# Optimization experiments

Measured on AMD Instinct MI355X. Metric: run time of the kernel, lower is better.

## Reference

```python
import jax, jax.numpy as jnp
import numpy as np

B, S = 2048, 256
V, E, H, LAT, NL = 4, 8, 64, 3, 2
NT = V + 2          # vocab + start + pad tokens
START = V
TEMP = 1.0


def setup_inputs() -> dict:
    key = jax.random.key(0)
    ks = jax.random.split(key, 32)
    def p(k, shape, scale=0.1):
        return jax.random.normal(k, shape, jnp.float32) * scale
    return {
        "tokens": jax.random.randint(ks[0], (B, S), 0, V),
        "emb": p(ks[1], (NT, E)),
        "enc_Wih0": p(ks[2], (3 * H, E)), "enc_Whh0": p(ks[3], (3 * H, H)),
        "enc_bih0": p(ks[4], (3 * H,)), "enc_bhh0": p(ks[5], (3 * H,)),
        "enc_Wih1": p(ks[6], (3 * H, H)), "enc_Whh1": p(ks[7], (3 * H, H)),
        "enc_bih1": p(ks[8], (3 * H,)), "enc_bhh1": p(ks[9], (3 * H,)),
        "fc_mu_W": p(ks[10], (LAT, H)), "fc_mu_b": p(ks[11], (LAT,)),
        "fc_var_W": p(ks[12], (LAT, H)), "fc_var_b": p(ks[13], (LAT,)),
        "dec_emb": p(ks[14], (NT, H)),
        "proj_W": p(ks[15], (H, LAT)), "proj_b": p(ks[16], (H,)),
        "dec_Wih0": p(ks[17], (3 * H, H)), "dec_Whh0": p(ks[18], (3 * H, H)),
        "dec_bih0": p(ks[19], (3 * H,)), "dec_bhh0": p(ks[20], (3 * H,)),
        "dec_Wih1": p(ks[21], (3 * H, H)), "dec_Whh1": p(ks[22], (3 * H, H)),
        "dec_bih1": p(ks[23], (3 * H,)), "dec_bhh1": p(ks[24], (3 * H,)),
        "head_W": p(ks[25], (V, H)), "head_b": p(ks[26], (V,)),
    }


def gru_cell(h, x, Wih, Whh, bih, bhh):
    # PyTorch GRU gate order: reset, update, new
    gi = x @ Wih.T + bih            # [B, 3H]
    gh = h @ Whh.T + bhh            # [B, 3H]
    ir, iz, ig = jnp.split(gi, 3, axis=-1)
    hr, hz, hg = jnp.split(gh, 3, axis=-1)
    r = jax.nn.sigmoid(ir + hr)
    z = jax.nn.sigmoid(iz + hz)
    n = jnp.tanh(ig + r * hg)
    return (1.0 - z) * n + z * h


def run_gru_layer(x, Wih, Whh, bih, bhh):
    # x: [B, S, D] -> (outputs [B, S, H], final hidden [B, H])
    def step(h, xt):
        h2 = gru_cell(h, xt, Wih, Whh, bih, bhh)
        return h2, h2
    h0 = jnp.zeros((x.shape[0], Whh.shape[1]), x.dtype)
    hT, ys = jax.lax.scan(step, h0, x.transpose(1, 0, 2))
    return ys.transpose(1, 0, 2), hT


def reference(tokens, emb, enc_Wih0, enc_Whh0, enc_bih0, enc_bhh0,
              enc_Wih1, enc_Whh1, enc_bih1, enc_bhh1,
              fc_mu_W, fc_mu_b, fc_var_W, fc_var_b,
              dec_emb, proj_W, proj_b,
              dec_Wih0, dec_Whh0, dec_bih0, dec_bhh0,
              dec_Wih1, dec_Whh1, dec_bih1, dec_bhh1,
              head_W, head_b):
    b, s = tokens.shape
    # ---- encode ----
    x = emb[tokens]                                   # [B, S, E]
    seq, _ = run_gru_layer(x, enc_Wih0, enc_Whh0, enc_bih0, enc_bhh0)
    _, h_last = run_gru_layer(seq, enc_Wih1, enc_Whh1, enc_bih1, enc_bhh1)
    mu = h_last @ fc_mu_W.T + fc_mu_b                 # [B, LAT]
    log_var = h_last @ fc_var_W.T + fc_var_b          # [B, LAT]
    # ---- reparameterize ----
    eps = jax.random.normal(jax.random.key(1), mu.shape, mu.dtype)
    z = eps * jnp.exp(0.5 * log_var) + mu
    hz = z @ proj_W.T + proj_b                        # [B, H]; same init for both layers
    tok0 = jnp.full((b,), START, jnp.int32)
    keys = jax.random.split(jax.random.key(2), s)
    def step(carry, k):
        h0, h1, tok = carry
        xe = dec_emb[tok]                             # [B, H]
        h0n = gru_cell(h0, xe, dec_Wih0, dec_Whh0, dec_bih0, dec_bhh0)
        h1n = gru_cell(h1, h0n, dec_Wih1, dec_Whh1, dec_bih1, dec_bhh1)
        logits = (h1n @ head_W.T + head_b) / TEMP     # [B, V]
        probs = jax.nn.softmax(logits, axis=-1)
        nt = jax.random.categorical(k, logits)        # multinomial sample (detached)
        return (h0n, h1n, nt), probs
    _, probs_seq = jax.lax.scan(step, (hz, hz, tok0), keys)   # [S, B, V]
    recons = probs_seq.transpose(1, 0, 2)[:, :, None, :]      # [B, S, 1, V]
    return recons, tokens, mu, log_var
```

## Files before the change

kernel.cpp:

```cpp
#include <hip/hip_runtime.h>
#include <stdint.h>

typedef unsigned int u32;
typedef unsigned short u16;

#define NB   2048
#define SS   256
#define HH   64
#define VV   4
#define LATD 3
#define NTHR 512

#define TOK_OFF (NB*SS*VV)
#define MU_OFF  (TOK_OFF + NB*SS)
#define LV_OFF  (MU_OFF + NB*LATD)

__device__ __forceinline__ void tf2x32(u32 k0, u32 k1, u32 x0, u32 x1, u32& o0, u32& o1){
  u32 k2 = k0 ^ k1 ^ 0x1BD11BDAu;
  x0 += k0; x1 += k1;
#define TFR(r) { x0 += x1; x1 = (x1<<r)|(x1>>(32-r)); x1 ^= x0; }
  TFR(13) TFR(15) TFR(26) TFR(6)   x0 += k1; x1 += k2 + 1u;
  TFR(17) TFR(29) TFR(16) TFR(24)  x0 += k2; x1 += k0 + 2u;
  TFR(13) TFR(15) TFR(26) TFR(6)   x0 += k0; x1 += k1 + 3u;
  TFR(17) TFR(29) TFR(16) TFR(24)  x0 += k1; x1 += k2 + 4u;
  TFR(13) TFR(15) TFR(26) TFR(6)   x0 += k2; x1 += k0 + 5u;
#undef TFR
  o0 = x0; o1 = x1;
}
__device__ __forceinline__ u32 foldb(u32 k0, u32 k1, u32 i){
  u32 a,b; tf2x32(k0,k1,0u,i,a,b); return a^b;
}
__device__ __forceinline__ float b2u(u32 bits){
  union{u32 i;float f;}c; c.i = (bits>>9) | 0x3f800000u; return c.f - 1.0f;
}
__device__ __forceinline__ float erfinv_f(float x){
  float w = -log1pf(-x*x);
  float p;
  if (w < 5.0f){
    w -= 2.5f;
    p = 2.81022636e-08f;
    p = fmaf(p,w, 3.43273939e-07f);
    p = fmaf(p,w,-3.5233877e-06f);
    p = fmaf(p,w,-4.39150654e-06f);
    p = fmaf(p,w, 0.00021858087f);
    p = fmaf(p,w,-0.00125372503f);
    p = fmaf(p,w,-0.00417768164f);
    p = fmaf(p,w, 0.246640727f);
    p = fmaf(p,w, 1.50140941f);
  } else {
    w = sqrtf(w) - 3.0f;
    p = -0.000200214257f;
    p = fmaf(p,w, 0.000100950558f);
    p = fmaf(p,w, 0.00134934322f);
    p = fmaf(p,w,-0.00367342844f);
    p = fmaf(p,w, 0.00573950773f);
    p = fmaf(p,w,-0.0076224613f);
    p = fmaf(p,w, 0.00943887047f);
    p = fmaf(p,w, 1.00167406f);
    p = fmaf(p,w, 2.83297682f);
  }
  return p*x;
}
__device__ __forceinline__ float sigm(float x){ return 1.0f/(1.0f+expf(-x)); }
__device__ __forceinline__ float rl(float x, int l){
  return __int_as_float(__builtin_amdgcn_readlane(__float_as_int(x), l));
}
__device__ __forceinline__ float wred(float x){
  #pragma unroll
  for (int m=1; m<64; m<<=1) x += __shfl_xor(x, m, 64);
  return x;
}

#define MATVEC1R(Wr, Wz, Wn, xv, ar, az, an)                                   \
  _Pragma("unroll")                                                            \
  for (int k4 = 0; k4 < 16; k4++){                                             \
    float4 wr = Wr[k4];                                                        \
    float4 wz = Wz[k4];                                                        \
    float4 wn = Wn[k4];                                                        \
    float x0 = rl(xv, 4*k4), x1 = rl(xv, 4*k4+1), x2 = rl(xv, 4*k4+2), x3 = rl(xv, 4*k4+3); \
    ar = fmaf(wr.x,x0,ar); ar = fmaf(wr.y,x1,ar); ar = fmaf(wr.z,x2,ar); ar = fmaf(wr.w,x3,ar); \
    az = fmaf(wz.x,x0,az); az = fmaf(wz.y,x1,az); az = fmaf(wz.z,x2,az); az = fmaf(wz.w,x3,az); \
    an = fmaf(wn.x,x0,an); an = fmaf(wn.y,x1,an); an = fmaf(wn.z,x2,an); an = fmaf(wn.w,x3,an); \
  }

#define MATVEC1L(W, xv, ar, az, an)                                            \
  _Pragma("unroll 2")                                                          \
  for (int k4 = 0; k4 < 16; k4++){                                             \
    float4 wr = W[k4*192 + j];                                                 \
    float4 wz = W[k4*192 + 64 + j];                                            \
    float4 wn = W[k4*192 + 128 + j];                                           \
    float x0 = rl(xv, 4*k4), x1 = rl(xv, 4*k4+1), x2 = rl(xv, 4*k4+2), x3 = rl(xv, 4*k4+3); \
    ar = fmaf(wr.x,x0,ar); ar = fmaf(wr.y,x1,ar); ar = fmaf(wr.z,x2,ar); ar = fmaf(wr.w,x3,ar); \
    az = fmaf(wz.x,x0,az); az = fmaf(wz.y,x1,az); az = fmaf(wz.z,x2,az); az = fmaf(wz.w,x3,az); \
    an = fmaf(wn.x,x0,an); an = fmaf(wn.y,x1,an); an = fmaf(wn.z,x2,an); an = fmaf(wn.w,x3,an); \
  }

#define LOAD_REG_W(G, Ar, Az, An)                                              \
  _Pragma("unroll")                                                            \
  for (int k4 = 0; k4 < 16; k4++){                                             \
    Ar[k4] = G[(j)*16 + k4];                                                   \
    Az[k4] = G[(64 + j)*16 + k4];                                              \
    An[k4] = G[(128 + j)*16 + k4];                                             \
  }

#define PIN4(v) asm volatile("" : "+v"(v.x), "+v"(v.y), "+v"(v.z), "+v"(v.w))
#define PIN_W(Ar, Az, An)                                                      \
  _Pragma("unroll")                                                            \
  for (int k4 = 0; k4 < 16; k4++){ PIN4(Ar[k4]); PIN4(Az[k4]); PIN4(An[k4]); }

__global__ __launch_bounds__(NTHR, 2) void enc_kernel(
    const int* __restrict__ tokens, const float* __restrict__ emb,
    const float* __restrict__ Wih0, const float* __restrict__ Whh0,
    const float* __restrict__ bih0, const float* __restrict__ bhh0,
    const float* __restrict__ Wih1, const float* __restrict__ Whh1,
    const float* __restrict__ bih1, const float* __restrict__ bhh1,
    const float* __restrict__ muW, const float* __restrict__ mub,
    const float* __restrict__ vaW, const float* __restrict__ vab,
    const float* __restrict__ pW,  const float* __restrict__ pb,
    float* __restrict__ out, float* __restrict__ hz_ws)
{
  __shared__ float4 wi1[16*192];
  __shared__ float4 wh1[16*192];
  __shared__ float tokT[VV*192];

  const int tid = threadIdx.x;
  const int b0  = blockIdx.x * 8;
  const int j   = tid & 63;
  const int wv  = tid >> 6;
  const int row = b0 + wv;

  for (int i4 = tid; i4 < 3072; i4 += NTHR){
    int g = i4 >> 4, k4 = i4 & 15;
    wi1[k4*192 + g] = ((const float4*)Wih1)[i4];
    wh1[k4*192 + g] = ((const float4*)Whh1)[i4];
  }
  if (tid < 192){
    #pragma unroll
    for (int v = 0; v < VV; v++){
      float acc = 0.0f;
      #pragma unroll
      for (int e = 0; e < 8; e++) acc = fmaf(emb[v*8+e], Wih0[tid*8+e], acc);
      tokT[v*192 + tid] = acc + bih0[tid];
    }
  }
  for (int i = tid; i < 8*SS; i += NTHR){
    int rr = i >> 8, tq = i & 255;
    out[TOK_OFF + (b0+rr)*SS + tq] = (float)tokens[(b0+rr)*SS + tq];
  }

  float4 w0r[16], w0z[16], w0n[16];
  {
    const float4* G0 = (const float4*)Whh0;
    LOAD_REG_W(G0, w0r, w0z, w0n)
    PIN_W(w0r, w0z, w0n)
  }
  __syncthreads();

  const float bhr0 = bhh0[j], bhz0 = bhh0[64+j], bhn0 = bhh0[128+j];
  const float bir1 = bih1[j], biz1 = bih1[64+j], bin1 = bih1[128+j];
  const float bhr1 = bhh1[j], bhz1 = bhh1[64+j], bhn1 = bhh1[128+j];

  float h0 = 0.0f, h1 = 0.0f;
  const int tR = row*SS;

  for (int t = 0; t < SS; t++){
    asm volatile("" ::: "memory");
    int k = tokens[tR + t];
    float ar=0, az=0, an=0;
    MATVEC1R(w0r, w0z, w0n, h0, ar, az, an)
    {
      float ir = tokT[k*192+j], iz = tokT[k*192+64+j], ig = tokT[k*192+128+j];
      float rg = sigm(ir + ar + bhr0);
      float zg = sigm(iz + az + bhz0);
      float ng = tanhf(ig + rg*(an + bhn0));
      h0 = (1.0f - zg)*ng + zg*h0;
    }
    float air=0, aiz=0, ain=0, ahr=0, ahz=0, ahn=0;
    MATVEC1L(wi1, h0, air, aiz, ain)
    MATVEC1L(wh1, h1, ahr, ahz, ahn)
    {
      float rg = sigm(air + bir1 + ahr + bhr1);
      float zg = sigm(aiz + biz1 + ahz + bhz1);
      float ng = tanhf(ain + bin1 + rg*(ahn + bhn1));
      h1 = (1.0f - zg)*ng + zg*h1;
    }
  }

  const float LO_ = -0.99999994f;
  {
    float hv = h1;
    int gb = row;
    float mu0,mu1,mu2, lv0,lv1,lv2;
    { float pm = muW[0*64+j]*hv; pm = wred(pm); mu0 = pm + mub[0];
      float pv = vaW[0*64+j]*hv; pv = wred(pv); lv0 = pv + vab[0]; }
    { float pm = muW[1*64+j]*hv; pm = wred(pm); mu1 = pm + mub[1];
      float pv = vaW[1*64+j]*hv; pv = wred(pv); lv1 = pv + vab[1]; }
    { float pm = muW[2*64+j]*hv; pm = wred(pm); mu2 = pm + mub[2];
      float pv = vaW[2*64+j]*hv; pv = wred(pv); lv2 = pv + vab[2]; }
    if (j < 3){
      float mv  = (j==0)?mu0:(j==1)?mu1:mu2;
      float lvv = (j==0)?lv0:(j==1)?lv1:lv2;
      out[MU_OFF + gb*LATD + j] = mv;
      out[LV_OFF + gb*LATD + j] = lvv;
    }
    float z0,z1,z2;
    #pragma unroll
    for (int l = 0; l < 3; l++){
      u32 bits = foldb(0u, 1u, (u32)(gb*LATD + l));
      float u01 = b2u(bits);
      float uu = u01 * 2.0f;
      uu = uu + LO_;
      uu = fmaxf(LO_, uu);
      float ep = 1.41421354f * erfinv_f(uu);
      float lvv = (l==0)?lv0:(l==1)?lv1:lv2;
      float mvv = (l==0)?mu0:(l==1)?mu1:mu2;
      float zv = ep * expf(0.5f*lvv) + mvv;
      if (l==0) z0 = zv; else if (l==1) z1 = zv; else z2 = zv;
    }
    float hzj = pW[j*3+0]*z0;
    hzj += pW[j*3+1]*z1;
    hzj += pW[j*3+2]*z2;
    hzj += pb[j];
    hz_ws[gb*HH + j] = hzj;
  }
}

__global__ __launch_bounds__(NTHR, 2) void dec_kernel(
    const float* __restrict__ demb,
    const float* __restrict__ Wih0, const float* __restrict__ Whh0,
    const float* __restrict__ bih0, const float* __restrict__ bhh0,
    const float* __restrict__ Wih1, const float* __restrict__ Whh1,
    const float* __restrict__ bih1, const float* __restrict__ bhh1,
    const float* __restrict__ headW, const float* __restrict__ headb,
    const float* __restrict__ hz_ws, float* __restrict__ out)
{
  __shared__ float4 wi1[16*192];
  __shared__ float4 wh1[16*192];
  __shared__ float decT[6*192];
  __shared__ u32 sk0[SS], sk1[SS];

  const int tid = threadIdx.x;
  const int b0  = blockIdx.x * 8;
  const int j   = tid & 63;
  const int wv  = tid >> 6;
  const int row = b0 + wv;

  for (int i4 = tid; i4 < 3072; i4 += NTHR){
    int g = i4 >> 4, k4 = i4 & 15;
    wi1[k4*192 + g] = ((const float4*)Wih1)[i4];
    wh1[k4*192 + g] = ((const float4*)Whh1)[i4];
  }
  if (tid < 192){
    #pragma unroll
    for (int v = 0; v < 6; v++){
      float acc = 0.0f;
      #pragma unroll 8
      for (int k = 0; k < 64; k++) acc = fmaf(demb[v*64+k], Wih0[tid*64+k], acc);
      decT[v*192 + tid] = acc + bih0[tid];
    }
  }
  if (tid < SS){
    u32 a,b; tf2x32(0u, 2u, 0u, (u32)tid, a, b);
    sk0[tid] = a; sk1[tid] = b;
  }

  float4 w0r[16], w0z[16], w0n[16];
  {
    const float4* G0 = (const float4*)Whh0;
    LOAD_REG_W(G0, w0r, w0z, w0n)
  }
  __syncthreads();

  const float bhr0 = bhh0[j], bhz0 = bhh0[64+j], bhn0 = bhh0[128+j];
  const float bir1 = bih1[j], biz1 = bih1[64+j], bin1 = bih1[128+j];
  const float bhr1 = bhh1[j], bhz1 = bhh1[64+j], bhn1 = bhh1[128+j];
  const float hw0 = headW[0*64+j], hw1 = headW[1*64+j], hw2 = headW[2*64+j], hw3 = headW[3*64+j];
  const float hb0 = headb[0], hb1 = headb[1], hb2 = headb[2], hb3 = headb[3];

  float h0 = hz_ws[row*HH + j];
  float h1 = h0;
  int tk = 4;

  const int vv = j & 3;
  const float TINY = 1.17549435e-38f;

  for (int t = 0; t < SS; t++){
    asm volatile("" ::: "memory");
    float ar=0, az=0, an=0;
    MATVEC1R(w0r, w0z, w0n, h0, ar, az, an)
    {
      float ir = decT[tk*192+j], iz = decT[tk*192+64+j], ig = decT[tk*192+128+j];
      float rg = sigm(ir + ar + bhr0);
      float zg = sigm(iz + az + bhz0);
      float ng = tanhf(ig + rg*(an + bhn0));
      h0 = (1.0f - zg)*ng + zg*h0;
    }
    float air=0, aiz=0, ain=0, ahr=0, ahz=0, ahn=0;
    MATVEC1L(wi1, h0, air, aiz, ain)
    MATVEC1L(wh1, h1, ahr, ahz, ahn)
    {
      float rg = sigm(air + bir1 + ahr + bhr1);
      float zg = sigm(aiz + biz1 + ahz + bhz1);
      float ng = tanhf(ain + bin1 + rg*(ahn + bhn1));
      h1 = (1.0f - zg)*ng + zg*h1;
    }
    float l0 = wred(hw0*h1) + hb0;
    float l1 = wred(hw1*h1) + hb1;
    float l2 = wred(hw2*h1) + hb2;
    float l3 = wred(hw3*h1) + hb3;
    float lg = (vv==0)?l0:(vv==1)?l1:(vv==2)?l2:l3;
    u32 bits = foldb(sk0[t], sk1[t], (u32)(row*VV + vv));
    float u01 = b2u(bits);
    float u = u01 + TINY;
    u = fmaxf(TINY, u);
    float gmb = -logf(-logf(u));
    float prt = lg + gmb;
    float mx = lg;
    mx = fmaxf(mx, __shfl_xor(mx, 1, 64));
    mx = fmaxf(mx, __shfl_xor(mx, 2, 64));
    float e = expf(lg - mx);
    float se = e;
    se += __shfl_xor(se, 1, 64);
    se += __shfl_xor(se, 2, 64);
    float prob = e / se;
    float bp = prt; int bv = vv;
    { float o = __shfl_xor(bp, 1, 64); int ov = __shfl_xor(bv, 1, 64);
      if (o > bp || (o == bp && ov < bv)){ bp = o; bv = ov; } }
    { float o = __shfl_xor(bp, 2, 64); int ov = __shfl_xor(bv, 2, 64);
      if (o > bp || (o == bp && ov < bv)){ bp = o; bv = ov; } }
    if (j < 4) out[(size_t)row*SS*VV + (size_t)t*VV + vv] = prob;
    tk = __builtin_amdgcn_readlane(bv, 0);
  }
}

extern "C" void kernel_launch(void* const* d_in, const int* in_sizes, int n_in,
                              void* d_out, int out_size, void* d_ws, size_t ws_size,
                              hipStream_t stream){
  const int*   tokens = (const int*)d_in[0];
  const float* emb    = (const float*)d_in[1];
  const float* eWih0  = (const float*)d_in[2];  const float* eWhh0 = (const float*)d_in[3];
  const float* ebih0  = (const float*)d_in[4];  const float* ebhh0 = (const float*)d_in[5];
  const float* eWih1  = (const float*)d_in[6];  const float* eWhh1 = (const float*)d_in[7];
  const float* ebih1  = (const float*)d_in[8];  const float* ebhh1 = (const float*)d_in[9];
  const float* muW    = (const float*)d_in[10]; const float* mub   = (const float*)d_in[11];
  const float* vaW    = (const float*)d_in[12]; const float* vab   = (const float*)d_in[13];
  const float* demb   = (const float*)d_in[14];
  const float* pW     = (const float*)d_in[15]; const float* pb    = (const float*)d_in[16];
  const float* dWih0  = (const float*)d_in[17]; const float* dWhh0 = (const float*)d_in[18];
  const float* dbih0  = (const float*)d_in[19]; const float* dbhh0 = (const float*)d_in[20];
  const float* dWih1  = (const float*)d_in[21]; const float* dWhh1 = (const float*)d_in[22];
  const float* dbih1  = (const float*)d_in[23]; const float* dbhh1 = (const float*)d_in[24];
  const float* hWp    = (const float*)d_in[25]; const float* hbp   = (const float*)d_in[26];
  float* out = (float*)d_out;
  float* hz = (float*)d_ws;

  enc_kernel<<<NB/8, NTHR, 0, stream>>>(tokens, emb,
      eWih0, eWhh0, ebih0, ebhh0, eWih1, eWhh1, ebih1, ebhh1,
      muW, mub, vaW, vab, pW, pb, out, hz);
  dec_kernel<<<NB/8, NTHR, 0, stream>>>(demb,
      dWih0, dWhh0, dbih0, dbhh0, dWih1, dWhh1, dbih1, dbhh1,
      hWp, hbp, hz, out);
}
```

Baseline: 2.632 ms.

## Split GRU matvecs across wave pairs by K-half, processing two rows per wave

Each pair of waves now handles two batch rows together. Each wave keeps only half of the layer-0 recurrent weights in registers and computes partial matvecs over its half of K. The partials are exchanged through shared memory with block-wide barriers, and in the decoder the sampled tokens are shared the same way. This halves register pressure for the pinned weights and reuses each weight load for two rows. In exchange it adds two __syncthreads per timestep plus extra LDS traffic and duplicated gate math.

```diff
diff --git a/kernel.cpp b/kernel.cpp
--- a/kernel.cpp
+++ b/kernel.cpp
@@ -2,7 +2,6 @@
 #include <stdint.h>
 
 typedef unsigned int u32;
-typedef unsigned short u16;
 
 #define NB   2048
 #define SS   256
@@ -71,42 +70,50 @@
   return x;
 }
 
-#define MATVEC1R(Wr, Wz, Wn, xv, ar, az, an)                                   \
+#define PIN4(v) asm volatile("" : "+v"(v.x), "+v"(v.y), "+v"(v.z), "+v"(v.w))
+#define PIN_W8(Ar, Az, An)                                                     \
   _Pragma("unroll")                                                            \
-  for (int k4 = 0; k4 < 16; k4++){                                             \
-    float4 wr = Wr[k4];                                                        \
-    float4 wz = Wz[k4];                                                        \
-    float4 wn = Wn[k4];                                                        \
-    float x0 = rl(xv, 4*k4), x1 = rl(xv, 4*k4+1), x2 = rl(xv, 4*k4+2), x3 = rl(xv, 4*k4+3); \
-    ar = fmaf(wr.x,x0,ar); ar = fmaf(wr.y,x1,ar); ar = fmaf(wr.z,x2,ar); ar = fmaf(wr.w,x3,ar); \
-    az = fmaf(wz.x,x0,az); az = fmaf(wz.y,x1,az); az = fmaf(wz.z,x2,az); az = fmaf(wz.w,x3,az); \
-    an = fmaf(wn.x,x0,an); an = fmaf(wn.y,x1,an); an = fmaf(wn.z,x2,an); an = fmaf(wn.w,x3,an); \
-  }
-
-#define MATVEC1L(W, xv, ar, az, an)                                            \
+  for (int k4 = 0; k4 < 8; k4++){ PIN4(Ar[k4]); PIN4(An[k4]); PIN4(Az[k4]); }
+
+#define MATVEC0P(hA, hB)                                                       \
+  _Pragma("unroll")                                                            \
+  for (int k4 = 0; k4 < 8; k4++){                                              \
+    float4 wr = w0r[k4], wz = w0z[k4], wn = w0n[k4];                           \
+    int kb = kb0 + 4*k4;                                                       \
+    float a0=rl(hA,kb), a1=rl(hA,kb+1), a2=rl(hA,kb+2), a3=rl(hA,kb+3);        \
+    float c0=rl(hB,kb), c1=rl(hB,kb+1), c2=rl(hB,kb+2), c3=rl(hB,kb+3);        \
+    arA=fmaf(wr.x,a0,arA); arA=fmaf(wr.y,a1,arA); arA=fmaf(wr.z,a2,arA); arA=fmaf(wr.w,a3,arA); \
+    azA=fmaf(wz.x,a0,azA); azA=fmaf(wz.y,a1,azA); azA=fmaf(wz.z,a2,azA); azA=fmaf(wz.w,a3,azA); \
+    anA=fmaf(wn.x,a0,anA); anA=fmaf(wn.y,a1,anA); anA=fmaf(wn.z,a2,anA); anA=fmaf(wn.w,a3,anA); \
+    arB=fmaf(wr.x,c0,arB); arB=fmaf(wr.y,c1,arB); arB=fmaf(wr.z,c2,arB); arB=fmaf(wr.w,c3,arB); \
+    azB=fmaf(wz.x,c0,azB); azB=fmaf(wz.y,c1,azB); azB=fmaf(wz.z,c2,azB); azB=fmaf(wz.w,c3,azB); \
+    anB=fmaf(wn.x,c0,anB); anB=fmaf(wn.y,c1,anB); anB=fmaf(wn.z,c2,anB); anB=fmaf(wn.w,c3,anB); \
+  }
+
+#define MATVEC1P(xA, xB, yA, yB)                                               \
   _Pragma("unroll 2")                                                          \
-  for (int k4 = 0; k4 < 16; k4++){                                             \
-    float4 wr = W[k4*192 + j];                                                 \
-    float4 wz = W[k4*192 + 64 + j];                                            \
-    float4 wn = W[k4*192 + 128 + j];                                           \
-    float x0 = rl(xv, 4*k4), x1 = rl(xv, 4*k4+1), x2 = rl(xv, 4*k4+2), x3 = rl(xv, 4*k4+3); \
-    ar = fmaf(wr.x,x0,ar); ar = fmaf(wr.y,x1,ar); ar = fmaf(wr.z,x2,ar); ar = fmaf(wr.w,x3,ar); \
-    az = fmaf(wz.x,x0,az); az = fmaf(wz.y,x1,az); az = fmaf(wz.z,x2,az); az = fmaf(wz.w,x3,az); \
-    an = fmaf(wn.x,x0,an); an = fmaf(wn.y,x1,an); an = fmaf(wn.z,x2,an); an = fmaf(wn.w,x3,an); \
-  }
-
-#define LOAD_REG_W(G, Ar, Az, An)                                              \
-  _Pragma("unroll")                                                            \
-  for (int k4 = 0; k4 < 16; k4++){                                             \
-    Ar[k4] = G[(j)*16 + k4];                                                   \
-    Az[k4] = G[(64 + j)*16 + k4];                                              \
-    An[k4] = G[(128 + j)*16 + k4];                                             \
-  }
-
-#define PIN4(v) asm volatile("" : "+v"(v.x), "+v"(v.y), "+v"(v.z), "+v"(v.w))
-#define PIN_W(Ar, Az, An)                                                      \
-  _Pragma("unroll")                                                            \
-  for (int k4 = 0; k4 < 16; k4++){ PIN4(Ar[k4]); PIN4(Az[k4]); PIN4(An[k4]); }
+  for (int k4 = 0; k4 < 8; k4++){                                              \
+    int ki = kh8 + k4;                                                         \
+    float4 wir = wi1[ki*192 + j],  wiz = wi1[ki*192 + 64 + j],  win = wi1[ki*192 + 128 + j]; \
+    float4 whr = wh1[ki*192 + j],  whz = wh1[ki*192 + 64 + j],  whn = wh1[ki*192 + 128 + j]; \
+    int kb = 4*ki;                                                             \
+    float xa0=rl(xA,kb), xa1=rl(xA,kb+1), xa2=rl(xA,kb+2), xa3=rl(xA,kb+3);    \
+    float xb0=rl(xB,kb), xb1=rl(xB,kb+1), xb2=rl(xB,kb+2), xb3=rl(xB,kb+3);    \
+    float ya0=rl(yA,kb), ya1=rl(yA,kb+1), ya2=rl(yA,kb+2), ya3=rl(yA,kb+3);    \
+    float yb0=rl(yB,kb), yb1=rl(yB,kb+1), yb2=rl(yB,kb+2), yb3=rl(yB,kb+3);    \
+    srA=fmaf(wir.x,xa0,srA); srA=fmaf(wir.y,xa1,srA); srA=fmaf(wir.z,xa2,srA); srA=fmaf(wir.w,xa3,srA); \
+    srA=fmaf(whr.x,ya0,srA); srA=fmaf(whr.y,ya1,srA); srA=fmaf(whr.z,ya2,srA); srA=fmaf(whr.w,ya3,srA); \
+    szA=fmaf(wiz.x,xa0,szA); szA=fmaf(wiz.y,xa1,szA); szA=fmaf(wiz.z,xa2,szA); szA=fmaf(wiz.w,xa3,szA); \
+    szA=fmaf(whz.x,ya0,szA); szA=fmaf(whz.y,ya1,szA); szA=fmaf(whz.z,ya2,szA); szA=fmaf(whz.w,ya3,szA); \
+    inA=fmaf(win.x,xa0,inA); inA=fmaf(win.y,xa1,inA); inA=fmaf(win.z,xa2,inA); inA=fmaf(win.w,xa3,inA); \
+    hnA=fmaf(whn.x,ya0,hnA); hnA=fmaf(whn.y,ya1,hnA); hnA=fmaf(whn.z,ya2,hnA); hnA=fmaf(whn.w,ya3,hnA); \
+    srB=fmaf(wir.x,xb0,srB); srB=fmaf(wir.y,xb1,srB); srB=fmaf(wir.z,xb2,srB); srB=fmaf(wir.w,xb3,srB); \
+    srB=fmaf(whr.x,yb0,srB); srB=fmaf(whr.y,yb1,srB); srB=fmaf(whr.z,yb2,srB); srB=fmaf(whr.w,yb3,srB); \
+    szB=fmaf(wiz.x,xb0,szB); szB=fmaf(wiz.y,xb1,szB); szB=fmaf(wiz.z,xb2,szB); szB=fmaf(wiz.w,xb3,szB); \
+    szB=fmaf(whz.x,yb0,szB); szB=fmaf(whz.y,yb1,szB); szB=fmaf(whz.z,yb2,szB); szB=fmaf(whz.w,yb3,szB); \
+    inB=fmaf(win.x,xb0,inB); inB=fmaf(win.y,xb1,inB); inB=fmaf(win.z,xb2,inB); inB=fmaf(win.w,xb3,inB); \
+    hnB=fmaf(whn.x,yb0,hnB); hnB=fmaf(whn.y,yb1,hnB); hnB=fmaf(whn.z,yb2,hnB); hnB=fmaf(whn.w,yb3,hnB); \
+  }
 
 __global__ __launch_bounds__(NTHR, 2) void enc_kernel(
     const int* __restrict__ tokens, const float* __restrict__ emb,
@@ -122,12 +129,22 @@
   __shared__ float4 wi1[16*192];
   __shared__ float4 wh1[16*192];
   __shared__ float tokT[VV*192];
+  __shared__ float4 ex1a[8][64];
+  __shared__ float2 ex1b[8][64];
+  __shared__ float4 ex2a[8][64];
+  __shared__ float4 ex2b[8][64];
 
   const int tid = threadIdx.x;
   const int b0  = blockIdx.x * 8;
   const int j   = tid & 63;
   const int wv  = tid >> 6;
-  const int row = b0 + wv;
+  const int kh  = wv & 1;
+  const int pw  = wv ^ 1;
+  const int rA  = b0 + (wv & ~1);
+  const int rB  = rA + 1;
+  const int rD  = b0 + wv;
+  const int kh8 = kh * 8;
+  const int kb0 = kh * 32;
 
   for (int i4 = tid; i4 < 3072; i4 += NTHR){
     int g = i4 >> 4, k4 = i4 & 15;
@@ -148,48 +165,77 @@
     out[TOK_OFF + (b0+rr)*SS + tq] = (float)tokens[(b0+rr)*SS + tq];
   }
 
-  float4 w0r[16], w0z[16], w0n[16];
+  float4 w0r[8], w0z[8], w0n[8];
   {
     const float4* G0 = (const float4*)Whh0;
-    LOAD_REG_W(G0, w0r, w0z, w0n)
-    PIN_W(w0r, w0z, w0n)
+    #pragma unroll
+    for (int k4 = 0; k4 < 8; k4++){
+      w0r[k4] = G0[(j)*16      + kh8 + k4];
+      w0z[k4] = G0[(64 + j)*16 + kh8 + k4];
+      w0n[k4] = G0[(128 + j)*16+ kh8 + k4];
+    }
+    PIN_W8(w0r, w0z, w0n)
   }
   __syncthreads();
 
   const float bhr0 = bhh0[j], bhz0 = bhh0[64+j], bhn0 = bhh0[128+j];
-  const float bir1 = bih1[j], biz1 = bih1[64+j], bin1 = bih1[128+j];
-  const float bhr1 = bhh1[j], bhz1 = bhh1[64+j], bhn1 = bhh1[128+j];
-
-  float h0 = 0.0f, h1 = 0.0f;
-  const int tR = row*SS;
+  const float bR1  = bih1[j]      + bhh1[j];
+  const float bZ1  = bih1[64+j]   + bhh1[64+j];
+  const float bin1 = bih1[128+j], bhn1 = bhh1[128+j];
+
+  float h0A = 0.0f, h0B = 0.0f, h1A = 0.0f, h1B = 0.0f;
 
   for (int t = 0; t < SS; t++){
     asm volatile("" ::: "memory");
-    int k = tokens[tR + t];
-    float ar=0, az=0, an=0;
-    MATVEC1R(w0r, w0z, w0n, h0, ar, az, an)
-    {
-      float ir = tokT[k*192+j], iz = tokT[k*192+64+j], ig = tokT[k*192+128+j];
-      float rg = sigm(ir + ar + bhr0);
-      float zg = sigm(iz + az + bhz0);
-      float ng = tanhf(ig + rg*(an + bhn0));
-      h0 = (1.0f - zg)*ng + zg*h0;
-    }
-    float air=0, aiz=0, ain=0, ahr=0, ahz=0, ahn=0;
-    MATVEC1L(wi1, h0, air, aiz, ain)
-    MATVEC1L(wh1, h1, ahr, ahz, ahn)
-    {
-      float rg = sigm(air + bir1 + ahr + bhr1);
-      float zg = sigm(aiz + biz1 + ahz + bhz1);
-      float ng = tanhf(ain + bin1 + rg*(ahn + bhn1));
-      h1 = (1.0f - zg)*ng + zg*h1;
+    int kA = tokens[rA*SS + t];
+    int kB = tokens[rB*SS + t];
+    float arA=0, azA=0, anA=0, arB=0, azB=0, anB=0;
+    MATVEC0P(h0A, h0B)
+    ex1a[wv][j] = make_float4(arA, azA, anA, arB);
+    ex1b[wv][j] = make_float2(azB, anB);
+    __syncthreads();
+    {
+      float4 qa = ex1a[pw][j]; float2 qb = ex1b[pw][j];
+      arA += qa.x; azA += qa.y; anA += qa.z;
+      arB += qa.w; azB += qb.x; anB += qb.y;
+    }
+    {
+      float ir = tokT[kA*192+j], iz = tokT[kA*192+64+j], ig = tokT[kA*192+128+j];
+      float rg = sigm(ir + arA + bhr0);
+      float zg = sigm(iz + azA + bhz0);
+      float ng = tanhf(ig + rg*(anA + bhn0));
+      h0A = (1.0f - zg)*ng + zg*h0A;
+    }
+    {
+      float ir = tokT[kB*192+j], iz = tokT[kB*192+64+j], ig = tokT[kB*192+128+j];
+      float rg = sigm(ir + arB + bhr0);
+      float zg = sigm(iz + azB + bhz0);
+      float ng = tanhf(ig + rg*(anB + bhn0));
+      h0B = (1.0f - zg)*ng + zg*h0B;
+    }
+    float srA=0, szA=0, inA=0, hnA=0, srB=0, szB=0, inB=0, hnB=0;
+    MATVEC1P(h0A, h0B, h1A, h1B)
+    ex2a[wv][j] = make_float4(srA, szA, inA, hnA);
+    ex2b[wv][j] = make_float4(srB, szB, inB, hnB);
+    __syncthreads();
+    {
+      float4 pa = ex2a[pw][j];
+      float rg = sigm(srA + pa.x + bR1);
+      float zg = sigm(szA + pa.y + bZ1);
+      float ng = tanhf(inA + pa.z + bin1 + rg*(hnA + pa.w + bhn1));
+      h1A = (1.0f - zg)*ng + zg*h1A;
+      float4 pb = ex2b[pw][j];
+      rg = sigm(srB + pb.x + bR1);
+      zg = sigm(szB + pb.y + bZ1);
+      ng = tanhf(inB + pb.z + bin1 + rg*(hnB + pb.w + bhn1));
+      h1B = (1.0f - zg)*ng + zg*h1B;
     }
   }
 
   const float LO_ = -0.99999994f;
   {
-    float hv = h1;
-    int gb = row;
+    float hv = kh ? h1B : h1A;
+    int gb = rD;
     float mu0,mu1,mu2, lv0,lv1,lv2;
     { float pm = muW[0*64+j]*hv; pm = wred(pm); mu0 = pm + mub[0];
       float pv = vaW[0*64+j]*hv; pv = wred(pv); lv0 = pv + vab[0]; }
@@ -238,12 +284,24 @@
   __shared__ float4 wh1[16*192];
   __shared__ float decT[6*192];
   __shared__ u32 sk0[SS], sk1[SS];
+  __shared__ int tokS[8];
+  __shared__ float4 ex1a[8][64];
+  __shared__ float2 ex1b[8][64];
+  __shared__ float4 ex2a[8][64];
+  __shared__ float4 ex2b[8][64];
 
   const int tid = threadIdx.x;
   const int b0  = blockIdx.x * 8;
   const int j   = tid & 63;
   const int wv  = tid >> 6;
-  const int row = b0 + wv;
+  const int kh  = wv & 1;
+  const int pw  = wv ^ 1;
+  const int rA  = b0 + (wv & ~1);
+  const int rB  = rA + 1;
+  const int rD  = b0 + wv;
+  const int kh8 = kh * 8;
+  const int kb0 = kh * 32;
+  const int pbase = wv & ~1;
 
   for (int i4 = tid; i4 < 3072; i4 += NTHR){
     int g = i4 >> 4, k4 = i4 & 15;
@@ -263,53 +321,87 @@
     u32 a,b; tf2x32(0u, 2u, 0u, (u32)tid, a, b);
     sk0[tid] = a; sk1[tid] = b;
   }
-
-  float4 w0r[16], w0z[16], w0n[16];
+  if (tid < 8) tokS[tid] = 4;
+
+  float4 w0r[8], w0z[8], w0n[8];
   {
     const float4* G0 = (const float4*)Whh0;
-    LOAD_REG_W(G0, w0r, w0z, w0n)
+    #pragma unroll
+    for (int k4 = 0; k4 < 8; k4++){
+      w0r[k4] = G0[(j)*16      + kh8 + k4];
+      w0z[k4] = G0[(64 + j)*16 + kh8 + k4];
+      w0n[k4] = G0[(128 + j)*16+ kh8 + k4];
+    }
+    PIN_W8(w0r, w0z, w0n)
   }
   __syncthreads();
 
   const float bhr0 = bhh0[j], bhz0 = bhh0[64+j], bhn0 = bhh0[128+j];
-  const float bir1 = bih1[j], biz1 = bih1[64+j], bin1 = bih1[128+j];
-  const float bhr1 = bhh1[j], bhz1 = bhh1[64+j], bhn1 = bhh1[128+j];
+  const float bR1  = bih1[j]      + bhh1[j];
+  const float bZ1  = bih1[64+j]   + bhh1[64+j];
+  const float bin1 = bih1[128+j], bhn1 = bhh1[128+j];
   const float hw0 = headW[0*64+j], hw1 = headW[1*64+j], hw2 = headW[2*64+j], hw3 = headW[3*64+j];
   const float hb0 = headb[0], hb1 = headb[1], hb2 = headb[2], hb3 = headb[3];
 
-  float h0 = hz_ws[row*HH + j];
-  float h1 = h0;
-  int tk = 4;
+  float h0A = hz_ws[rA*HH + j];
+  float h0B = hz_ws[rB*HH + j];
+  float h1A = h0A, h1B = h0B;
 
   const int vv = j & 3;
   const float TINY = 1.17549435e-38f;
 
   for (int t = 0; t < SS; t++){
     asm volatile("" ::: "memory");
-    float ar=0, az=0, an=0;
-    MATVEC1R(w0r, w0z, w0n, h0, ar, az, an)
-    {
-      float ir = decT[tk*192+j], iz = decT[tk*192+64+j], ig = decT[tk*192+128+j];
-      float rg = sigm(ir + ar + bhr0);
-      float zg = sigm(iz + az + bhz0);
-      float ng = tanhf(ig + rg*(an + bhn0));
-      h0 = (1.0f - zg)*ng + zg*h0;
-    }
-    float air=0, aiz=0, ain=0, ahr=0, ahz=0, ahn=0;
-    MATVEC1L(wi1, h0, air, aiz, ain)
-    MATVEC1L(wh1, h1, ahr, ahz, ahn)
-    {
-      float rg = sigm(air + bir1 + ahr + bhr1);
-      float zg = sigm(aiz + biz1 + ahz + bhz1);
-      float ng = tanhf(ain + bin1 + rg*(ahn + bhn1));
-      h1 = (1.0f - zg)*ng + zg*h1;
-    }
-    float l0 = wred(hw0*h1) + hb0;
-    float l1 = wred(hw1*h1) + hb1;
-    float l2 = wred(hw2*h1) + hb2;
-    float l3 = wred(hw3*h1) + hb3;
+    float arA=0, azA=0, anA=0, arB=0, azB=0, anB=0;
+    MATVEC0P(h0A, h0B)
+    ex1a[wv][j] = make_float4(arA, azA, anA, arB);
+    ex1b[wv][j] = make_float2(azB, anB);
+    __syncthreads();
+    int tkA = tokS[pbase];
+    int tkB = tokS[pbase+1];
+    {
+      float4 qa = ex1a[pw][j]; float2 qb = ex1b[pw][j];
+      arA += qa.x; azA += qa.y; anA += qa.z;
+      arB += qa.w; azB += qb.x; anB += qb.y;
+    }
+    {
+      float ir = decT[tkA*192+j], iz = decT[tkA*192+64+j], ig = decT[tkA*192+128+j];
+      float rg = sigm(ir + arA + bhr0);
+      float zg = sigm(iz + azA + bhz0);
+      float ng = tanhf(ig + rg*(anA + bhn0));
+      h0A = (1.0f - zg)*ng + zg*h0A;
+    }
+    {
+      float ir = decT[tkB*192+j], iz = decT[tkB*192+64+j], ig = decT[tkB*192+128+j];
+      float rg = sigm(ir + arB + bhr0);
+      float zg = sigm(iz + azB + bhz0);
+      float ng = tanhf(ig + rg*(anB + bhn0));
+      h0B = (1.0f - zg)*ng + zg*h0B;
+    }
+    float srA=0, szA=0, inA=0, hnA=0, srB=0, szB=0, inB=0, hnB=0;
+    MATVEC1P(h0A, h0B, h1A, h1B)
+    ex2a[wv][j] = make_float4(srA, szA, inA, hnA);
+    ex2b[wv][j] = make_float4(srB, szB, inB, hnB);
+    __syncthreads();
+    {
+      float4 pa = ex2a[pw][j];
+      float rg = sigm(srA + pa.x + bR1);
+      float zg = sigm(szA + pa.y + bZ1);
+      float ng = tanhf(inA + pa.z + bin1 + rg*(hnA + pa.w + bhn1));
+      h1A = (1.0f - zg)*ng + zg*h1A;
+      float4 pb = ex2b[pw][j];
+      rg = sigm(srB + pb.x + bR1);
+      zg = sigm(szB + pb.y + bZ1);
+      ng = tanhf(inB + pb.z + bin1 + rg*(hnB + pb.w + bhn1));
+      h1B = (1.0f - zg)*ng + zg*h1B;
+    }
+    float hD = kh ? h1B : h1A;
+    float l0 = wred(hw0*hD) + hb0;
+    float l1 = wred(hw1*hD) + hb1;
+    float l2 = wred(hw2*hD) + hb2;
+    float l3 = wred(hw3*hD) + hb3;
     float lg = (vv==0)?l0:(vv==1)?l1:(vv==2)?l2:l3;
-    u32 bits = foldb(sk0[t], sk1[t], (u32)(row*VV + vv));
+    u32 bits = foldb(sk0[t], sk1[t], (u32)(rD*VV + vv));
     float u01 = b2u(bits);
     float u = u01 + TINY;
     u = fmaxf(TINY, u);
@@ -328,8 +420,9 @@
       if (o > bp || (o == bp && ov < bv)){ bp = o; bv = ov; } }
     { float o = __shfl_xor(bp, 2, 64); int ov = __shfl_xor(bv, 2, 64);
       if (o > bp || (o == bp && ov < bv)){ bp = o; bv = ov; } }
-    if (j < 4) out[(size_t)row*SS*VV + (size_t)t*VV + vv] = prob;
-    tk = __builtin_amdgcn_readlane(bv, 0);
+    if (j < 4) out[(size_t)rD*SS*VV + (size_t)t*VV + vv] = prob;
+    int tkD = __builtin_amdgcn_readlane(bv, 0);
+    if (j == 0) tokS[wv] = tkD;
   }
 }
 
```

After: 2.928 ms. +11.2%, slower.
